# Performance work log

Measured on AMD Instinct MI355X. Metric: run time of the kernel, lower is better.

## Reference

```python
import jax, jax.numpy as jnp
import numpy as np

D = 256      # d_model
K = 8        # knn neighbors
Q = 2048     # num queries
N = 32768    # num superpoints
H = 8        # mamba heads (d_inner/head_dim)
HD = 64      # head_dim
ST = 64      # state_size
DIN = H * HD                 # 512, expand*d_model
CONV = DIN + 2 * ST          # 640
NPROJ = 2 * DIN + 2 * ST + H # 1160
HID = 1024   # ffn hidden
NL = 2       # ssm layers
KC = 4       # conv kernel


def _ln(x, eps=1e-5):
    m = x.mean(-1, keepdims=True)
    v = ((x - m) ** 2).mean(-1, keepdims=True)
    return (x - m) * jax.lax.rsqrt(v + eps)


def _silu(x):
    return x * jax.nn.sigmoid(x)


def _mamba2(x, Win, Wconv, bconv, A_log, Dh, dtb, rmsw, Wout):
    # x: [B, L, D]; faithful HF Mamba2Mixer recurrent form
    B, L, _ = x.shape
    proj = x @ Win.T  # [B,L,NPROJ]
    z, xBC, dt = jnp.split(proj, [DIN, DIN + CONV], axis=-1)
    # causal depthwise conv1d, kernel KC, left pad KC-1
    xp = jnp.pad(xBC, ((0, 0), (KC - 1, 0), (0, 0)))
    conv = sum(xp[:, j:j + L, :] * Wconv[:, j] for j in range(KC))
    xBC = _silu(conv + bconv)
    xs, Bm, Cm = jnp.split(xBC, [DIN, DIN + ST], axis=-1)
    dt = jax.nn.softplus(dt + dtb)  # [B,L,H]
    A = -jnp.exp(A_log)             # [H]
    xh = xs.reshape(B, L, H, HD)
    dA = jnp.exp(dt * A)            # [B,L,H]
    dBx = dt[..., None, None] * Bm[:, :, None, None, :] * xh[..., None]  # [B,L,H,HD,ST]

    def step(h, inp):
        dA_t, dBx_t, C_t = inp
        h = h * dA_t[..., None, None] + dBx_t
        y = jnp.einsum('bhds,bs->bhd', h, C_t)
        return h, y

    h0 = jnp.zeros((B, H, HD, ST), x.dtype)
    _, ys = jax.lax.scan(step, h0, (dA.transpose(1, 0, 2),
                                    dBx.transpose(1, 0, 2, 3, 4),
                                    Cm.transpose(1, 0, 2)))
    y = ys.transpose(1, 0, 2, 3) + Dh[None, None, :, None] * xh
    y = y.reshape(B, L, DIN) * _silu(z)  # gated RMSNorm
    y = y * jax.lax.rsqrt((y * y).mean(-1, keepdims=True) + 1e-5) * rmsw
    return y @ Wout.T


def setup_inputs() -> dict:
    key = jax.random.key(0)
    ks = jax.random.split(key, 32)
    s = 0.02
    rn = lambda i, sh: jax.random.normal(ks[i], sh, jnp.float32) * s
    inp = {
        'query': jax.random.normal(ks[0], (Q, D), jnp.float32),
        'query_pos': jax.random.uniform(ks[1], (Q, 3), jnp.float32),
        'inst_feats': jax.random.normal(ks[2], (N, D), jnp.float32),
        'sp_coords': jax.random.uniform(ks[3], (N, 3), jnp.float32),
        'w_q': rn(4, (D, D)), 'w_v': rn(5, (D, D)), 'w_o': rn(6, (D, D)),
        'w_k': rn(7, (K, D)), 'w_b': jnp.zeros((K,), jnp.float32),
        'ssm_Win': rn(8, (NL, NPROJ, D)),
        'ssm_Wconv': rn(9, (NL, CONV, KC)),
        'ssm_bconv': jnp.zeros((NL, CONV), jnp.float32),
        'ssm_Alog': jnp.log(jnp.broadcast_to(jnp.arange(1, H + 1, dtype=jnp.float32), (NL, H))),
        'ssm_D': jnp.ones((NL, H), jnp.float32),
        'ssm_dtb': jax.random.uniform(ks[10], (NL, H), jnp.float32) * 0.1,
        'ssm_rmsw': jnp.ones((NL, DIN), jnp.float32),
        'ssm_Wout': rn(11, (NL, D, DIN)),
        'ffn_w1': rn(12, (HID, D)), 'ffn_b1': jnp.zeros((HID,), jnp.float32),
        'ffn_w2': rn(13, (D, HID)), 'ffn_b2': jnp.zeros((D,), jnp.float32),
        'order': jnp.stack([jax.random.permutation(ks[14], Q),
                            jax.random.permutation(ks[15], Q)]).astype(jnp.int32),
    }
    return inp


def reference(query, query_pos, inst_feats, sp_coords,
              w_q, w_v, w_o, w_k, w_b,
              ssm_Win, ssm_Wconv, ssm_bconv, ssm_Alog, ssm_D, ssm_dtb, ssm_rmsw, ssm_Wout,
              ffn_w1, ffn_b1, ffn_w2, ffn_b2, order):
    # --- MambaAggregation: KNN group + small-K softmax mixing ---
    d2 = (query_pos ** 2).sum(-1, keepdims=True) + (sp_coords ** 2).sum(-1)[None, :] \
         - 2.0 * query_pos @ sp_coords.T  # [Q,N]
    _, idx = jax.lax.top_k(-d2, K)        # [Q,K] nearest neighbors
    feat = inst_feats[idx]                # [Q,K,D]
    q = query @ w_q.T
    v = feat @ w_v.T
    kw = jax.nn.softmax(q @ w_k.T + w_b, axis=-1)          # [Q,K]
    w = jnp.einsum('qk,qd,qkd->qd', kw, q, v)
    x = _ln(w @ w_o.T + query)

    # --- SSM: serialize along 2 orders, Mamba2 mix, unsort, average ---
    inv = jnp.argsort(order, axis=1)  # [2,Q]
    for l in range(NL):
        sc = x
        xn = _ln(x)
        xs = xn[order]  # [2,Q,D], two serialization paths as batch
        y = _mamba2(xs, ssm_Win[l], ssm_Wconv[l], ssm_bconv[l], ssm_Alog[l],
                    ssm_D[l], ssm_dtb[l], ssm_rmsw[l], ssm_Wout[l])
        back = jnp.take_along_axis(y, inv[:, :, None], axis=1)  # undo sort
        x = _ln(sc + back.mean(0))

    # --- FFN ---
    h = jax.nn.gelu(x @ ffn_w1.T + ffn_b1, approximate=False) @ ffn_w2.T + ffn_b2
    return _ln(x + h)
```

## Files before the change

kernel.cpp:

```cpp
#include <hip/hip_runtime.h>
#include <cstdint>


typedef __attribute__((ext_vector_type(8))) short bf16x8;
typedef __attribute__((ext_vector_type(4))) float f32x4;

__device__ __forceinline__ unsigned short f2bf(float f) {
  unsigned int u = __float_as_uint(f);
  u += 0x7fff + ((u >> 16) & 1);
  return (unsigned short)(u >> 16);
}
__device__ __forceinline__ float bf2f(unsigned short h) {
  return __uint_as_float(((unsigned int)h) << 16);
}

__global__ __launch_bounds__(256) void cvt_kernel(
    const float* __restrict__ src, unsigned short* __restrict__ hi,
    unsigned short* __restrict__ lo, int n4)
{
  const int i = blockIdx.x*256 + threadIdx.x;
  if (i < n4) {
    const float4 v = ((const float4*)src)[i];
    const unsigned short h0=f2bf(v.x), h1=f2bf(v.y), h2=f2bf(v.z), h3=f2bf(v.w);
    const unsigned short l0=f2bf(v.x-bf2f(h0)), l1=f2bf(v.y-bf2f(h1)),
                         l2=f2bf(v.z-bf2f(h2)), l3=f2bf(v.w-bf2f(h3));
    ((uint2*)hi)[i] = make_uint2((unsigned)h0 | ((unsigned)h1<<16),
                                 (unsigned)h2 | ((unsigned)h3<<16));
    ((uint2*)lo)[i] = make_uint2((unsigned)l0 | ((unsigned)l1<<16),
                                 (unsigned)l2 | ((unsigned)l3<<16));
  }
}

__device__ __forceinline__ bool flex_less(float d, int i, float dr, int ir) {
  return d < dr || (d == dr && i < ir);
}

#define KNN_INS_F(dv, iv)                                                      \
  do {                                                                         \
    const float _d = (dv); const int _v = (iv);                                \
    const bool a0 = _d < bd0;                                                  \
    const bool a1 = _d < bd1;                                                  \
    const bool a2 = _d < bd2;                                                  \
    const bool a3 = _d < bd3;                                                  \
    const bool a4 = _d < bd4;                                                  \
    const bool a5 = _d < bd5;                                                  \
    const bool a6 = _d < bd6;                                                  \
    bd7 = a6 ? bd6 : _d;              id7 = a6 ? id6 : _v;                     \
    bd6 = a5 ? bd5 : (a6 ? _d : bd6); id6 = a5 ? id5 : (a6 ? _v : id6);        \
    bd5 = a4 ? bd4 : (a5 ? _d : bd5); id5 = a4 ? id4 : (a5 ? _v : id5);        \
    bd4 = a3 ? bd3 : (a4 ? _d : bd4); id4 = a3 ? id3 : (a4 ? _v : id4);        \
    bd3 = a2 ? bd2 : (a3 ? _d : bd3); id3 = a2 ? id2 : (a3 ? _v : id3);        \
    bd2 = a1 ? bd1 : (a2 ? _d : bd2); id2 = a1 ? id1 : (a2 ? _v : id2);        \
    bd1 = a0 ? bd0 : (a1 ? _d : bd1); id1 = a0 ? id0 : (a1 ? _v : id1);        \
    bd0 = a0 ? _d : bd0;              id0 = a0 ? _v : id0;                     \
  } while (0)

#define KNN_INS_FLEX(dv, iv)                                                   \
  do {                                                                         \
    const float _d = (dv); const int _v = (iv);                                \
    const bool a0 = flex_less(_d, _v, bd0, id0);                               \
    const bool a1 = flex_less(_d, _v, bd1, id1);                               \
    const bool a2 = flex_less(_d, _v, bd2, id2);                               \
    const bool a3 = flex_less(_d, _v, bd3, id3);                               \
    const bool a4 = flex_less(_d, _v, bd4, id4);                               \
    const bool a5 = flex_less(_d, _v, bd5, id5);                               \
    const bool a6 = flex_less(_d, _v, bd6, id6);                               \
    bd7 = a6 ? bd6 : _d;              id7 = a6 ? id6 : _v;                     \
    bd6 = a5 ? bd5 : (a6 ? _d : bd6); id6 = a5 ? id5 : (a6 ? _v : id6);        \
    bd5 = a4 ? bd4 : (a5 ? _d : bd5); id5 = a4 ? id4 : (a5 ? _v : id5);        \
    bd4 = a3 ? bd3 : (a4 ? _d : bd4); id4 = a3 ? id3 : (a4 ? _v : id4);        \
    bd3 = a2 ? bd2 : (a3 ? _d : bd3); id3 = a2 ? id2 : (a3 ? _v : id3);        \
    bd2 = a1 ? bd1 : (a2 ? _d : bd2); id2 = a1 ? id1 : (a2 ? _v : id2);        \
    bd1 = a0 ? bd0 : (a1 ? _d : bd1); id1 = a0 ? id0 : (a1 ? _v : id1);        \
    bd0 = a0 ? _d : bd0;              id0 = a0 ? _v : id0;                     \
  } while (0)

#define KNN_RESET_F()                                                          \
  do {                                                                         \
    bd0=bd1=bd2=bd3=bd4=bd5=bd6=bd7 = 3.4e38f;                                 \
    id0=id1=id2=id3=id4=id5=id6=id7 = 0x7fffffff;                              \
  } while (0)

__global__ void prep_kernel(const float* __restrict__ spos,
                            float4* __restrict__ P4)
{
#pragma clang fp contract(off)
  const int n = blockIdx.x*256 + threadIdx.x;
  if (n < 32768) {
    const float sx = spos[n*3+0], sy = spos[n*3+1], sz = spos[n*3+2];
    P4[n] = make_float4(sx, sy, sz, sx*sx + sy*sy + sz*sz);
  }
}

__global__ __launch_bounds__(256) void knn_kernel(
    const float* __restrict__ qpos, const float4* __restrict__ P4,
    int* __restrict__ idx_out)
{
#pragma clang fp contract(off)
  __shared__ float skey[32];
  __shared__ int   sidx[32];
  const int q = blockIdx.x, tid = threadIdx.x;
  const int wave = tid >> 6, lane = tid & 63;
  const float qx = qpos[q*3+0], qy = qpos[q*3+1], qz = qpos[q*3+2];
  const float qq = qx*qx + qy*qy + qz*qz;
  float bd0,bd1,bd2,bd3,bd4,bd5,bd6,bd7;
  int   id0,id1,id2,id3,id4,id5,id6,id7;
  KNN_RESET_F();
  const float4* pp = P4 + (wave << 13) + lane;
  int nb = (wave << 13);
  for (int it = 0; it < 128; ++it) {
    const float4 p = *pp;  pp += 64;
    const float d2 = (qq + p.w) - 2.0f*(qx*p.x + qy*p.y + qz*p.z);
    unsigned long long m = __ballot(d2 < bd7);
    while (m) {
      const int l = __ffsll(m) - 1;
      m &= m - 1;
      const float dk = __shfl(d2, l);
      if (dk < bd7) KNN_INS_F(dk, nb + l);
    }
    nb += 64;
  }
  if (lane == 0) {
    const int o = wave*8;
    skey[o+0]=bd0; skey[o+1]=bd1; skey[o+2]=bd2; skey[o+3]=bd3;
    skey[o+4]=bd4; skey[o+5]=bd5; skey[o+6]=bd6; skey[o+7]=bd7;
    sidx[o+0]=id0; sidx[o+1]=id1; sidx[o+2]=id2; sidx[o+3]=id3;
    sidx[o+4]=id4; sidx[o+5]=id5; sidx[o+6]=id6; sidx[o+7]=id7;
  }
  __syncthreads();
  if (tid == 0) {
    KNN_RESET_F();
    for (int s = 0; s < 32; ++s) {
      const float dk = skey[s];
      const int   ui = sidx[s];
      if (flex_less(dk, ui, bd7, id7)) KNN_INS_FLEX(dk, ui);
    }
    idx_out[q*8+0]=id0; idx_out[q*8+1]=id1; idx_out[q*8+2]=id2; idx_out[q*8+3]=id3;
    idx_out[q*8+4]=id4; idx_out[q*8+5]=id5; idx_out[q*8+6]=id6; idx_out[q*8+7]=id7;
  }
}

__global__ void inv_kernel(const int* __restrict__ order, int* __restrict__ inv)
{
  int i = blockIdx.x*blockDim.x + threadIdx.x;
  if (i < 4096) { int b = i >> 11, t = i & 2047; inv[(b<<11) + order[i]] = t; }
}

#define GBM 128
#define GBN 128
#define GBK 32
#define GLDK 40
__global__ __launch_bounds__(256) void gemm_mfma(
    const unsigned short* __restrict__ Ahp, const unsigned short* __restrict__ Alp,
    const int* __restrict__ rowmap,
    const unsigned short* __restrict__ Bhp, const unsigned short* __restrict__ Blp,
    const float* __restrict__ bias,
    float* __restrict__ Y,
    unsigned short* __restrict__ Yh, unsigned short* __restrict__ Yl,
    int M, int Nn, int Kd, int act)
{
  __shared__ unsigned short Ah[GBM*GLDK], Al[GBM*GLDK];
  __shared__ unsigned short Bh[GBN*GLDK], Bl[GBN*GLDK];
  const int tid = threadIdx.x;
  const int bm = blockIdx.x, bn = blockIdx.y;
  const int wid = tid >> 6, lane = tid & 63;
  const int wr = wid >> 1, wc = wid & 1;
  const int l15 = lane & 15, lk = (lane >> 4) << 3;

  const int srow = tid >> 1, sk = (tid & 1) << 4;
  const int agrow = bm*GBM + srow;
  const int asrc = rowmap ? rowmap[agrow] : agrow;
  const unsigned short* ArH = Ahp + (size_t)asrc * Kd + sk;
  const unsigned short* ArL = Alp + (size_t)asrc * Kd + sk;
  const int wrow = bn*GBN + srow;
  const bool bok = (wrow < Nn);
  const unsigned short* BrH = Bhp + (size_t)(bok ? wrow : 0) * Kd + sk;
  const unsigned short* BrL = Blp + (size_t)(bok ? wrow : 0) * Kd + sk;

  f32x4 acc[4][4];
#pragma unroll
  for (int m = 0; m < 4; ++m)
#pragma unroll
    for (int n = 0; n < 4; ++n) acc[m][n] = (f32x4){0.f,0.f,0.f,0.f};

  const uint4 z4 = make_uint4(0u,0u,0u,0u);
  for (int k0 = 0; k0 < Kd; k0 += GBK) {
    const int so = srow*GLDK + sk;
    *(uint4*)&Ah[so]     = *(const uint4*)(ArH + k0);
    *(uint4*)&Ah[so + 8] = *(const uint4*)(ArH + k0 + 8);
    *(uint4*)&Al[so]     = *(const uint4*)(ArL + k0);
    *(uint4*)&Al[so + 8] = *(const uint4*)(ArL + k0 + 8);
    *(uint4*)&Bh[so]     = bok ? *(const uint4*)(BrH + k0)     : z4;
    *(uint4*)&Bh[so + 8] = bok ? *(const uint4*)(BrH + k0 + 8) : z4;
    *(uint4*)&Bl[so]     = bok ? *(const uint4*)(BrL + k0)     : z4;
    *(uint4*)&Bl[so + 8] = bok ? *(const uint4*)(BrL + k0 + 8) : z4;
    __syncthreads();
    bf16x8 afh[4], afl[4], bfh[4], bfl[4];
#pragma unroll
    for (int m = 0; m < 4; ++m) {
      const int row = wr*64 + m*16 + l15;
      afh[m] = *(const bf16x8*)&Ah[row*GLDK + lk];
      afl[m] = *(const bf16x8*)&Al[row*GLDK + lk];
    }
#pragma unroll
    for (int n = 0; n < 4; ++n) {
      const int row = wc*64 + n*16 + l15;
      bfh[n] = *(const bf16x8*)&Bh[row*GLDK + lk];
      bfl[n] = *(const bf16x8*)&Bl[row*GLDK + lk];
    }
#pragma unroll
    for (int m = 0; m < 4; ++m)
#pragma unroll
      for (int n = 0; n < 4; ++n) {
        acc[m][n] = __builtin_amdgcn_mfma_f32_16x16x32_bf16(afh[m], bfh[n], acc[m][n], 0,0,0);
        acc[m][n] = __builtin_amdgcn_mfma_f32_16x16x32_bf16(afh[m], bfl[n], acc[m][n], 0,0,0);
        acc[m][n] = __builtin_amdgcn_mfma_f32_16x16x32_bf16(afl[m], bfh[n], acc[m][n], 0,0,0);
      }
    __syncthreads();
  }
  const int crow0 = bm*GBM + wr*64 + (lane >> 4)*4;
#pragma unroll
  for (int m = 0; m < 4; ++m) {
#pragma unroll
    for (int n = 0; n < 4; ++n) {
      const int col = bn*GBN + wc*64 + n*16 + l15;
      if (col < Nn) {
#pragma unroll
        for (int r = 0; r < 4; ++r) {
          float v = acc[m][n][r];
          if (bias) v += bias[col];
          if (act == 1) v = 0.5f*v*(1.f + erff(v*0.7071067811865475f));
          const size_t idx = (size_t)(crow0 + m*16 + r)*Nn + col;
          if (Yh) {
            const unsigned short h = f2bf(v);
            Yh[idx] = h; Yl[idx] = f2bf(v - bf2f(h));
          } else {
            Y[idx] = v;
          }
        }
      }
    }
  }
}

__global__ __launch_bounds__(256) void kwmix_kernel(
    const float* __restrict__ QP, const float* __restrict__ wk,
    const float* __restrict__ wb, const float* __restrict__ V,
    unsigned short* __restrict__ Wh, unsigned short* __restrict__ Wl)
{
  const int wave = threadIdx.x >> 6, lane = threadIdx.x & 63;
  const int q = blockIdx.x*4 + wave;
  float qv[4];
#pragma unroll
  for (int j = 0; j < 4; ++j) qv[j] = QP[(size_t)q*256 + lane + 64*j];
  float logit[8];
#pragma unroll
  for (int k = 0; k < 8; ++k) {
    float p = 0.f;
#pragma unroll
    for (int j = 0; j < 4; ++j) p += qv[j]*wk[k*256 + lane + 64*j];
    for (int off = 32; off; off >>= 1) p += __shfl_xor(p, off);
    logit[k] = p + wb[k];
  }
  float mx = logit[0];
#pragma unroll
  for (int k = 1; k < 8; ++k) mx = fmaxf(mx, logit[k]);
  float e[8]; float s = 0.f;
#pragma unroll
  for (int k = 0; k < 8; ++k) { e[k] = expf(logit[k]-mx); s += e[k]; }
  float inv = 1.f/s;
  float acc[4] = {0.f,0.f,0.f,0.f};
#pragma unroll
  for (int k = 0; k < 8; ++k) {
    float kwv = e[k]*inv;
#pragma unroll
    for (int j = 0; j < 4; ++j)
      acc[j] = fmaf(kwv, V[(size_t)(q*8+k)*256 + lane + 64*j], acc[j]);
  }
#pragma unroll
  for (int j = 0; j < 4; ++j) {
    const float v = qv[j]*acc[j];
    const unsigned short h = f2bf(v);
    const size_t o = (size_t)q*256 + lane + 64*j;
    Wh[o] = h; Wl[o] = f2bf(v - bf2f(h));
  }
}

__global__ __launch_bounds__(256) void ln_kernel(
    const float* __restrict__ a, const float* __restrict__ b,
    float* __restrict__ out,
    unsigned short* __restrict__ oh, unsigned short* __restrict__ ol,
    int rows)
{
  const int wave = threadIdx.x >> 6, lane = threadIdx.x & 63;
  const int row = blockIdx.x*4 + wave;
  if (row >= rows) return;
  float v[4];
#pragma unroll
  for (int j = 0; j < 4; ++j) {
    float x = a[(size_t)row*256 + lane + 64*j];
    if (b) x += b[(size_t)row*256 + lane + 64*j];
    v[j] = x;
  }
  float s = v[0]+v[1]+v[2]+v[3];
  for (int off = 32; off; off >>= 1) s += __shfl_xor(s, off);
  float m = s * (1.0f/256.0f);
  float t = 0.f;
#pragma unroll
  for (int j = 0; j < 4; ++j) { float d = v[j]-m; t += d*d; }
  for (int off = 32; off; off >>= 1) t += __shfl_xor(t, off);
  float r = rsqrtf(t * (1.0f/256.0f) + 1e-5f);
#pragma unroll
  for (int j = 0; j < 4; ++j) {
    const float y = (v[j]-m)*r;
    const size_t o = (size_t)row*256 + lane + 64*j;
    if (out) out[o] = y;
    if (oh) { const unsigned short h = f2bf(y); oh[o] = h; ol[o] = f2bf(y - bf2f(h)); }
  }
}

__global__ __launch_bounds__(256) void ln_unsort_kernel(
    const float* __restrict__ OUTL, const int* __restrict__ INV,
    float* __restrict__ X,
    unsigned short* __restrict__ oh, unsigned short* __restrict__ ol)
{
  const int wave = threadIdx.x >> 6, lane = threadIdx.x & 63;
  const int q = blockIdx.x*4 + wave;
  const int i0 = INV[q], i1 = INV[2048 + q];
  float v[4];
#pragma unroll
  for (int j = 0; j < 4; ++j) {
    int d = lane + 64*j;
    v[j] = X[(size_t)q*256 + d]
         + 0.5f*(OUTL[(size_t)i0*256 + d] + OUTL[(size_t)(2048+i1)*256 + d]);
  }
  float s = v[0]+v[1]+v[2]+v[3];
  for (int off = 32; off; off >>= 1) s += __shfl_xor(s, off);
  float m = s * (1.0f/256.0f);
  float t = 0.f;
#pragma unroll
  for (int j = 0; j < 4; ++j) { float d = v[j]-m; t += d*d; }
  for (int off = 32; off; off >>= 1) t += __shfl_xor(t, off);
  float r = rsqrtf(t * (1.0f/256.0f) + 1e-5f);
#pragma unroll
  for (int j = 0; j < 4; ++j) {
    const float y = (v[j]-m)*r;
    const size_t o = (size_t)q*256 + lane + 64*j;
    X[o] = y;
    if (oh) { const unsigned short h = f2bf(y); oh[o] = h; ol[o] = f2bf(y - bf2f(h)); }
  }
}

__global__ void conv_kernel(const float* __restrict__ PROJ,
    const float* __restrict__ Wc, const float* __restrict__ bc,
    float* __restrict__ XBC)
{
  const int c = threadIdx.x;
  const int bt = blockIdx.x;
  const int t = bt & 2047;
  float acc = bc[c];
#pragma unroll
  for (int j = 0; j < 4; ++j) {
    int d = j - 3;
    if (t + d >= 0)
      acc = fmaf(PROJ[(size_t)(bt + d)*1160 + 512 + c], Wc[c*4+j], acc);
  }
  XBC[(size_t)bt*640 + c] = acc / (1.f + expf(-acc));
}

__global__ void dta_kernel(const float* __restrict__ PROJ,
    const float* __restrict__ dtb, const float* __restrict__ Alog,
    float* __restrict__ Ddt, float* __restrict__ Dda)
{
  const int i = blockIdx.x*256 + threadIdx.x;
  const int bt = i >> 3, hh = i & 7;
  float x = PROJ[(size_t)bt*1160 + 1152 + hh] + dtb[hh];
  float dt = (x > 20.f) ? x : log1pf(expf(x));
  float A = -expf(Alog[hh]);
  Ddt[hh*4096 + bt] = dt;
  Dda[hh*4096 + bt] = expf(dt * A);
}

__global__ __launch_bounds__(64) void scan1_kernel(
    const float* __restrict__ XBC, const float* __restrict__ Ddt,
    const float* __restrict__ Dda, float* __restrict__ SCH, float* __restrict__ PC)
{
  const int blk = blockIdx.x;
  const int c = blk & 31, hh = (blk >> 5) & 7, b = blk >> 8;
  const int lane = threadIdx.x;
  const int t0 = (b << 11) + (c << 6);
  __shared__ float Bsh[64][64];
  __shared__ float Xsh[64][64];
  __shared__ float dAs[64], dts[64];
#pragma unroll
  for (int it = 0; it < 16; ++it) {
    int idx = it*64 + lane;
    int t = idx >> 4, c4 = (idx & 15) << 2;
    *(float4*)&Bsh[t][c4] = *(const float4*)&XBC[(size_t)(t0 + t)*640 + 512 + c4];
    *(float4*)&Xsh[t][c4] = *(const float4*)&XBC[(size_t)(t0 + t)*640 + (hh<<6) + c4];
  }
  dAs[lane] = Dda[hh*4096 + t0 + lane];
  dts[lane] = Ddt[hh*4096 + t0 + lane];
  __syncthreads();
  float h[64];
#pragma unroll
  for (int s = 0; s < 64; ++s) h[s] = 0.f;
  float p = 1.f;
  for (int t = 0; t < 64; ++t) {
    const float dA = dAs[t];
    const float u = dts[t]*Xsh[t][lane];
    p *= dA;
    const float4* B4 = (const float4*)&Bsh[t][0];
#pragma unroll
    for (int s4 = 0; s4 < 16; ++s4) {
      float4 bv = B4[s4];
      h[4*s4+0] = fmaf(h[4*s4+0], dA, bv.x*u);
      h[4*s4+1] = fmaf(h[4*s4+1], dA, bv.y*u);
      h[4*s4+2] = fmaf(h[4*s4+2], dA, bv.z*u);
      h[4*s4+3] = fmaf(h[4*s4+3], dA, bv.w*u);
    }
  }
  float* op = SCH + (size_t)blk*4096 + lane*64;
#pragma unroll
  for (int s4 = 0; s4 < 16; ++s4)
    ((float4*)op)[s4] = make_float4(h[4*s4], h[4*s4+1], h[4*s4+2], h[4*s4+3]);
  if (lane == 0) PC[blk] = p;
}

__global__ void combine_kernel(float* __restrict__ SCH, const float* __restrict__ PC)
{
  const int tid = blockIdx.x*256 + threadIdx.x;
  const int bh = tid >> 12, ds = tid & 4095;
  float h = 0.f;
  for (int cc = 0; cc < 32; ++cc) {
    size_t o = ((size_t)(bh*32 + cc) << 12) + ds;
    float s = SCH[o];
    SCH[o] = h;
    h = fmaf(h, PC[bh*32+cc], s);
  }
}

__global__ __launch_bounds__(64) void scan2_kernel(
    const float* __restrict__ XBC, const float* __restrict__ Ddt,
    const float* __restrict__ Dda, const float* __restrict__ HST,
    const float* __restrict__ Dm, float* __restrict__ Yout)
{
  const int blk = blockIdx.x;
  const int c = blk & 31, hh = (blk >> 5) & 7, b = blk >> 8;
  const int lane = threadIdx.x;
  const int t0 = (b << 11) + (c << 6);
  __shared__ float Bsh[64][64];
  __shared__ float Csh[64][64];
  __shared__ float Xsh[64][64];
  __shared__ float dAs[64], dts[64];
#pragma unroll
  for (int it = 0; it < 16; ++it) {
    int idx = it*64 + lane;
    int t = idx >> 4, c4 = (idx & 15) << 2;
    *(float4*)&Bsh[t][c4] = *(const float4*)&XBC[(size_t)(t0 + t)*640 + 512 + c4];
    *(float4*)&Csh[t][c4] = *(const float4*)&XBC[(size_t)(t0 + t)*640 + 576 + c4];
    *(float4*)&Xsh[t][c4] = *(const float4*)&XBC[(size_t)(t0 + t)*640 + (hh<<6) + c4];
  }
  dAs[lane] = Dda[hh*4096 + t0 + lane];
  dts[lane] = Ddt[hh*4096 + t0 + lane];
  const float Dh = Dm[hh];
  float h[64];
  const float4* hp = (const float4*)(HST + (size_t)blk*4096 + lane*64);
#pragma unroll
  for (int s4 = 0; s4 < 16; ++s4) {
    float4 t4 = hp[s4];
    h[4*s4+0]=t4.x; h[4*s4+1]=t4.y; h[4*s4+2]=t4.z; h[4*s4+3]=t4.w;
  }
  __syncthreads();
  for (int t = 0; t < 64; ++t) {
    const float dA = dAs[t];
    const float u = dts[t]*Xsh[t][lane];
    float y = 0.f;
    const float4* B4 = (const float4*)&Bsh[t][0];
    const float4* C4 = (const float4*)&Csh[t][0];
#pragma unroll
    for (int s4 = 0; s4 < 16; ++s4) {
      float4 bv = B4[s4];
      float4 cv = C4[s4];
      h[4*s4+0] = fmaf(h[4*s4+0], dA, bv.x*u); y = fmaf(cv.x, h[4*s4+0], y);
      h[4*s4+1] = fmaf(h[4*s4+1], dA, bv.y*u); y = fmaf(cv.y, h[4*s4+1], y);
      h[4*s4+2] = fmaf(h[4*s4+2], dA, bv.z*u); y = fmaf(cv.z, h[4*s4+2], y);
      h[4*s4+3] = fmaf(h[4*s4+3], dA, bv.w*u); y = fmaf(cv.w, h[4*s4+3], y);
    }
    Yout[(size_t)(t0 + t)*512 + (hh<<6) + lane] = y + Dh*Xsh[t][lane];
  }
}

__global__ __launch_bounds__(256) void gaterms_kernel(
    const float* __restrict__ Y, const float* __restrict__ PROJ,
    const float* __restrict__ rmsw,
    unsigned short* __restrict__ Oh, unsigned short* __restrict__ Ol)
{
  const int wave = threadIdx.x >> 6, lane = threadIdx.x & 63;
  const int row = blockIdx.x*4 + wave;
  float v[8]; float ss = 0.f;
#pragma unroll
  for (int j = 0; j < 8; ++j) {
    float y = Y[(size_t)row*512 + lane + 64*j];
    float z = PROJ[(size_t)row*1160 + lane + 64*j];
    float g = y * (z / (1.f + expf(-z)));
    v[j] = g; ss += g*g;
  }
  for (int off = 32; off; off >>= 1) ss += __shfl_xor(ss, off);
  float r = rsqrtf(ss * (1.0f/512.0f) + 1e-5f);
#pragma unroll
  for (int j = 0; j < 8; ++j) {
    const float o = v[j] * r * rmsw[lane + 64*j];
    const unsigned short h = f2bf(o);
    const size_t ix = (size_t)row*512 + lane + 64*j;
    Oh[ix] = h; Ol[ix] = f2bf(o - bf2f(h));
  }
}

extern "C" void kernel_launch(void* const* d_in, const int* in_sizes, int n_in,
                              void* d_out, int out_size, void* d_ws, size_t ws_size,
                              hipStream_t stream)
{
  (void)in_sizes; (void)n_in; (void)out_size; (void)ws_size;
  const float* query = (const float*)d_in[0];
  const float* qpos  = (const float*)d_in[1];
  const float* feats = (const float*)d_in[2];
  const float* spos  = (const float*)d_in[3];
  const float* w_q   = (const float*)d_in[4];
  const float* w_v   = (const float*)d_in[5];
  const float* w_o   = (const float*)d_in[6];
  const float* w_k   = (const float*)d_in[7];
  const float* w_b   = (const float*)d_in[8];
  const float* Win   = (const float*)d_in[9];
  const float* Wconv = (const float*)d_in[10];
  const float* bconv = (const float*)d_in[11];
  const float* Alog  = (const float*)d_in[12];
  const float* Dm    = (const float*)d_in[13];
  const float* dtb   = (const float*)d_in[14];
  const float* rmsw  = (const float*)d_in[15];
  const float* Wout  = (const float*)d_in[16];
  const float* fw1   = (const float*)d_in[17];
  const float* fb1   = (const float*)d_in[18];
  const float* fw2   = (const float*)d_in[19];
  const float* fb2   = (const float*)d_in[20];
  const int*   order = (const int*)d_in[21];
  float* out = (float*)d_out;

  char* ws = (char*)d_ws;
  size_t off = 0;
  auto alloc = [&](size_t bytes) -> void* {
    void* p = ws + off;
    off = (off + bytes + 255) & ~(size_t)255;
    return p;
  };
  int*   IDX = (int*)alloc((size_t)2048*8*4);
  int*   INV = (int*)alloc((size_t)4096*4);
  float* PC  = (float*)alloc((size_t)512*4);
  float4* P4 = (float4*)alloc((size_t)32768*16);
  float* Ddt = (float*)alloc((size_t)4096*8*4);
  float* Dda = (float*)alloc((size_t)4096*8*4);
  float* QP  = (float*)alloc((size_t)2048*256*4);
  float* WO  = (float*)alloc((size_t)2048*256*4);
  float* X   = (float*)alloc((size_t)2048*256*4);
  float* U1  = (float*)alloc((size_t)4096*1160*4);
  float* U2  = (float*)alloc((size_t)4096*640*4);
  float* SCH = (float*)alloc((size_t)512*4096*4);
  float* Yb  = (float*)alloc((size_t)4096*512*4);
  float* U6  = (float*)alloc((size_t)4096*256*4);
  unsigned short* Qh  = (unsigned short*)alloc((size_t)2048*256*2);
  unsigned short* Ql  = (unsigned short*)alloc((size_t)2048*256*2);
  unsigned short* U7h = (unsigned short*)alloc((size_t)32768*256*2);
  unsigned short* U7l = (unsigned short*)alloc((size_t)32768*256*2);
  unsigned short* WBh = (unsigned short*)alloc((size_t)2048*256*2);
  unsigned short* WBl = (unsigned short*)alloc((size_t)2048*256*2);
  unsigned short* XNh = (unsigned short*)alloc((size_t)2048*256*2);
  unsigned short* XNl = (unsigned short*)alloc((size_t)2048*256*2);
  unsigned short* Ybh = (unsigned short*)alloc((size_t)4096*512*2);
  unsigned short* Ybl = (unsigned short*)alloc((size_t)4096*512*2);
  unsigned short* Xh  = (unsigned short*)alloc((size_t)2048*256*2);
  unsigned short* Xl  = (unsigned short*)alloc((size_t)2048*256*2);
  unsigned short* Wqh = (unsigned short*)alloc((size_t)256*256*2);
  unsigned short* Wql = (unsigned short*)alloc((size_t)256*256*2);
  unsigned short* Wvh = (unsigned short*)alloc((size_t)256*256*2);
  unsigned short* Wvl = (unsigned short*)alloc((size_t)256*256*2);
  unsigned short* Woh = (unsigned short*)alloc((size_t)256*256*2);
  unsigned short* Wol = (unsigned short*)alloc((size_t)256*256*2);
  unsigned short* Wih = (unsigned short*)alloc((size_t)2*1160*256*2);
  unsigned short* Wil = (unsigned short*)alloc((size_t)2*1160*256*2);
  unsigned short* Wuh = (unsigned short*)alloc((size_t)2*256*512*2);
  unsigned short* Wul = (unsigned short*)alloc((size_t)2*256*512*2);
  unsigned short* F1h = (unsigned short*)alloc((size_t)1024*256*2);
  unsigned short* F1l = (unsigned short*)alloc((size_t)1024*256*2);
  unsigned short* F2h = (unsigned short*)alloc((size_t)256*1024*2);
  unsigned short* F2l = (unsigned short*)alloc((size_t)256*1024*2);
  float* Vb   = U1;  float* PROJ = U1;
  float* XBC  = U2;
  float* OUTL = U6;  float* FFO  = U6;
  unsigned short* FFHh = U7h;
  unsigned short* FFHl = U7l;

  auto cvt = [&](const float* s, unsigned short* h, unsigned short* l, int n) {
    cvt_kernel<<<(n/4 + 255)/256, 256, 0, stream>>>(s, h, l, n/4);
  };

  inv_kernel<<<16, 256, 0, stream>>>(order, INV);
  prep_kernel<<<128, 256, 0, stream>>>(spos, P4);
  knn_kernel<<<2048, 256, 0, stream>>>(qpos, P4, IDX);
  cvt(query, Qh, Ql, 2048*256);
  cvt(feats, U7h, U7l, 32768*256);
  cvt(w_q, Wqh, Wql, 256*256);
  cvt(w_v, Wvh, Wvl, 256*256);
  cvt(w_o, Woh, Wol, 256*256);
  cvt(Win, Wih, Wil, 2*1160*256);
  cvt(Wout, Wuh, Wul, 2*256*512);
  cvt(fw1, F1h, F1l, 1024*256);
  cvt(fw2, F2h, F2l, 256*1024);
  gemm_mfma<<<dim3(16,2), 256, 0, stream>>>(Qh, Ql, nullptr, Wqh, Wql, nullptr,
                                            QP, nullptr, nullptr, 2048,256,256,0);
  gemm_mfma<<<dim3(128,2), 256, 0, stream>>>(U7h, U7l, IDX, Wvh, Wvl, nullptr,
                                             Vb, nullptr, nullptr, 16384,256,256,0);
  kwmix_kernel<<<512, 256, 0, stream>>>(QP, w_k, w_b, Vb, WBh, WBl);
  gemm_mfma<<<dim3(16,2), 256, 0, stream>>>(WBh, WBl, nullptr, Woh, Wol, nullptr,
                                            WO, nullptr, nullptr, 2048,256,256,0);
  ln_kernel<<<512, 256, 0, stream>>>(WO, query, X, nullptr, nullptr, 2048);

  for (int l = 0; l < 2; ++l) {
    ln_kernel<<<512, 256, 0, stream>>>(X, nullptr, nullptr, XNh, XNl, 2048);
    gemm_mfma<<<dim3(32,10), 256, 0, stream>>>(XNh, XNl, order,
                                               Wih + (size_t)l*1160*256,
                                               Wil + (size_t)l*1160*256,
                                               nullptr, PROJ, nullptr, nullptr,
                                               4096,1160,256,0);
    conv_kernel<<<4096, 640, 0, stream>>>(PROJ, Wconv + l*640*4, bconv + l*640, XBC);
    dta_kernel<<<128, 256, 0, stream>>>(PROJ, dtb + l*8, Alog + l*8, Ddt, Dda);
    scan1_kernel<<<512, 64, 0, stream>>>(XBC, Ddt, Dda, SCH, PC);
    combine_kernel<<<256, 256, 0, stream>>>(SCH, PC);
    scan2_kernel<<<512, 64, 0, stream>>>(XBC, Ddt, Dda, SCH, Dm + l*8, Yb);
    gaterms_kernel<<<1024, 256, 0, stream>>>(Yb, PROJ, rmsw + l*512, Ybh, Ybl);
    gemm_mfma<<<dim3(32,2), 256, 0, stream>>>(Ybh, Ybl, nullptr,
                                              Wuh + (size_t)l*256*512,
                                              Wul + (size_t)l*256*512,
                                              nullptr, OUTL, nullptr, nullptr,
                                              4096,256,512,0);
    ln_unsort_kernel<<<512, 256, 0, stream>>>(OUTL, INV, X,
                                              (l==1) ? Xh : nullptr,
                                              (l==1) ? Xl : nullptr);
  }

  gemm_mfma<<<dim3(16,8), 256, 0, stream>>>(Xh, Xl, nullptr, F1h, F1l, fb1,
                                            nullptr, FFHh, FFHl, 2048,1024,256,1);
  gemm_mfma<<<dim3(16,2), 256, 0, stream>>>(FFHh, FFHl, nullptr, F2h, F2l, fb2,
                                            FFO, nullptr, nullptr, 2048,256,1024,0);
  ln_kernel<<<512, 256, 0, stream>>>(FFO, X, out, nullptr, nullptr, 2048);
}
```

Before: 658.9 us.

## Mix gathered features before V projection and halve GEMM N-tile

Uses linearity to reorder the aggregation: instead of projecting all 16384 gathered neighbor features through w_v and then mixing, the softmax weights first mix the raw fp32 features per query, then a 2048-row GEMM applies w_v and multiplies elementwise by q in its epilogue. This removes the conversion of the full 32768x256 feature table and the 16384-row V GEMM. The GEMM N-tile also shrinks from 128 to 64, doubling the grid to improve occupancy on small GEMMs. The trade-off is reordered fp32 summation and a new epilogue multiply operand.

```diff
diff --git a/kernel.cpp b/kernel.cpp
--- a/kernel.cpp
+++ b/kernel.cpp
@@ -147,14 +147,14 @@
 }
 
 #define GBM 128
-#define GBN 128
+#define GBN 64
 #define GBK 32
 #define GLDK 40
 __global__ __launch_bounds__(256) void gemm_mfma(
     const unsigned short* __restrict__ Ahp, const unsigned short* __restrict__ Alp,
     const int* __restrict__ rowmap,
     const unsigned short* __restrict__ Bhp, const unsigned short* __restrict__ Blp,
-    const float* __restrict__ bias,
+    const float* __restrict__ bias, const float* __restrict__ emul,
     float* __restrict__ Y,
     unsigned short* __restrict__ Yh, unsigned short* __restrict__ Yl,
     int M, int Nn, int Kd, int act)
@@ -167,35 +167,35 @@
   const int wr = wid >> 1, wc = wid & 1;
   const int l15 = lane & 15, lk = (lane >> 4) << 3;
 
-  const int srow = tid >> 1, sk = (tid & 1) << 4;
-  const int agrow = bm*GBM + srow;
+  const int sar = tid >> 1, sak = (tid & 1) << 4;
+  const int agrow = bm*GBM + sar;
   const int asrc = rowmap ? rowmap[agrow] : agrow;
-  const unsigned short* ArH = Ahp + (size_t)asrc * Kd + sk;
-  const unsigned short* ArL = Alp + (size_t)asrc * Kd + sk;
-  const int wrow = bn*GBN + srow;
+  const unsigned short* ArH = Ahp + (size_t)asrc * Kd + sak;
+  const unsigned short* ArL = Alp + (size_t)asrc * Kd + sak;
+  const int sbr = tid >> 2, sbk = (tid & 3) << 3;
+  const int wrow = bn*GBN + sbr;
   const bool bok = (wrow < Nn);
-  const unsigned short* BrH = Bhp + (size_t)(bok ? wrow : 0) * Kd + sk;
-  const unsigned short* BrL = Blp + (size_t)(bok ? wrow : 0) * Kd + sk;
-
-  f32x4 acc[4][4];
+  const unsigned short* BrH = Bhp + (size_t)(bok ? wrow : 0) * Kd + sbk;
+  const unsigned short* BrL = Blp + (size_t)(bok ? wrow : 0) * Kd + sbk;
+
+  f32x4 acc[4][2];
 #pragma unroll
   for (int m = 0; m < 4; ++m)
 #pragma unroll
-    for (int n = 0; n < 4; ++n) acc[m][n] = (f32x4){0.f,0.f,0.f,0.f};
+    for (int n = 0; n < 2; ++n) acc[m][n] = (f32x4){0.f,0.f,0.f,0.f};
 
   const uint4 z4 = make_uint4(0u,0u,0u,0u);
   for (int k0 = 0; k0 < Kd; k0 += GBK) {
-    const int so = srow*GLDK + sk;
-    *(uint4*)&Ah[so]     = *(const uint4*)(ArH + k0);
-    *(uint4*)&Ah[so + 8] = *(const uint4*)(ArH + k0 + 8);
-    *(uint4*)&Al[so]     = *(const uint4*)(ArL + k0);
-    *(uint4*)&Al[so + 8] = *(const uint4*)(ArL + k0 + 8);
-    *(uint4*)&Bh[so]     = bok ? *(const uint4*)(BrH + k0)     : z4;
-    *(uint4*)&Bh[so + 8] = bok ? *(const uint4*)(BrH + k0 + 8) : z4;
-    *(uint4*)&Bl[so]     = bok ? *(const uint4*)(BrL + k0)     : z4;
-    *(uint4*)&Bl[so + 8] = bok ? *(const uint4*)(BrL + k0 + 8) : z4;
+    const int ao = sar*GLDK + sak;
+    *(uint4*)&Ah[ao]     = *(const uint4*)(ArH + k0);
+    *(uint4*)&Ah[ao + 8] = *(const uint4*)(ArH + k0 + 8);
+    *(uint4*)&Al[ao]     = *(const uint4*)(ArL + k0);
+    *(uint4*)&Al[ao + 8] = *(const uint4*)(ArL + k0 + 8);
+    const int bo = sbr*GLDK + sbk;
+    *(uint4*)&Bh[bo] = bok ? *(const uint4*)(BrH + k0) : z4;
+    *(uint4*)&Bl[bo] = bok ? *(const uint4*)(BrL + k0) : z4;
     __syncthreads();
-    bf16x8 afh[4], afl[4], bfh[4], bfl[4];
+    bf16x8 afh[4], afl[4], bfh[2], bfl[2];
 #pragma unroll
     for (int m = 0; m < 4; ++m) {
       const int row = wr*64 + m*16 + l15;
@@ -203,15 +203,15 @@
       afl[m] = *(const bf16x8*)&Al[row*GLDK + lk];
     }
 #pragma unroll
-    for (int n = 0; n < 4; ++n) {
-      const int row = wc*64 + n*16 + l15;
+    for (int n = 0; n < 2; ++n) {
+      const int row = wc*32 + n*16 + l15;
       bfh[n] = *(const bf16x8*)&Bh[row*GLDK + lk];
       bfl[n] = *(const bf16x8*)&Bl[row*GLDK + lk];
     }
 #pragma unroll
     for (int m = 0; m < 4; ++m)
 #pragma unroll
-      for (int n = 0; n < 4; ++n) {
+      for (int n = 0; n < 2; ++n) {
         acc[m][n] = __builtin_amdgcn_mfma_f32_16x16x32_bf16(afh[m], bfh[n], acc[m][n], 0,0,0);
         acc[m][n] = __builtin_amdgcn_mfma_f32_16x16x32_bf16(afh[m], bfl[n], acc[m][n], 0,0,0);
         acc[m][n] = __builtin_amdgcn_mfma_f32_16x16x32_bf16(afl[m], bfh[n], acc[m][n], 0,0,0);
@@ -222,8 +222,8 @@
 #pragma unroll
   for (int m = 0; m < 4; ++m) {
 #pragma unroll
-    for (int n = 0; n < 4; ++n) {
-      const int col = bn*GBN + wc*64 + n*16 + l15;
+    for (int n = 0; n < 2; ++n) {
+      const int col = bn*GBN + wc*32 + n*16 + l15;
       if (col < Nn) {
 #pragma unroll
         for (int r = 0; r < 4; ++r) {
@@ -231,6 +231,7 @@
           if (bias) v += bias[col];
           if (act == 1) v = 0.5f*v*(1.f + erff(v*0.7071067811865475f));
           const size_t idx = (size_t)(crow0 + m*16 + r)*Nn + col;
+          if (emul) v *= emul[idx];
           if (Yh) {
             const unsigned short h = f2bf(v);
             Yh[idx] = h; Yl[idx] = f2bf(v - bf2f(h));
@@ -243,10 +244,11 @@
   }
 }
 
-__global__ __launch_bounds__(256) void kwmix_kernel(
+__global__ __launch_bounds__(256) void kwmix2_kernel(
     const float* __restrict__ QP, const float* __restrict__ wk,
-    const float* __restrict__ wb, const float* __restrict__ V,
-    unsigned short* __restrict__ Wh, unsigned short* __restrict__ Wl)
+    const float* __restrict__ wb, const float* __restrict__ feats,
+    const int* __restrict__ IDX,
+    unsigned short* __restrict__ Fh, unsigned short* __restrict__ Fl)
 {
   const int wave = threadIdx.x >> 6, lane = threadIdx.x & 63;
   const int q = blockIdx.x*4 + wave;
@@ -272,17 +274,17 @@
   float acc[4] = {0.f,0.f,0.f,0.f};
 #pragma unroll
   for (int k = 0; k < 8; ++k) {
-    float kwv = e[k]*inv;
+    const float kwv = e[k]*inv;
+    const int ii = IDX[q*8+k];
 #pragma unroll
     for (int j = 0; j < 4; ++j)
-      acc[j] = fmaf(kwv, V[(size_t)(q*8+k)*256 + lane + 64*j], acc[j]);
+      acc[j] = fmaf(kwv, feats[(size_t)ii*256 + lane + 64*j], acc[j]);
   }
 #pragma unroll
   for (int j = 0; j < 4; ++j) {
-    const float v = qv[j]*acc[j];
-    const unsigned short h = f2bf(v);
+    const unsigned short h = f2bf(acc[j]);
     const size_t o = (size_t)q*256 + lane + 64*j;
-    Wh[o] = h; Wl[o] = f2bf(v - bf2f(h));
+    Fh[o] = h; Fl[o] = f2bf(acc[j] - bf2f(h));
   }
 }
 
@@ -569,8 +571,8 @@
   float* U6  = (float*)alloc((size_t)4096*256*4);
   unsigned short* Qh  = (unsigned short*)alloc((size_t)2048*256*2);
   unsigned short* Ql  = (unsigned short*)alloc((size_t)2048*256*2);
-  unsigned short* U7h = (unsigned short*)alloc((size_t)32768*256*2);
-  unsigned short* U7l = (unsigned short*)alloc((size_t)32768*256*2);
+  unsigned short* U7h = (unsigned short*)alloc((size_t)2048*1024*2);
+  unsigned short* U7l = (unsigned short*)alloc((size_t)2048*1024*2);
   unsigned short* WBh = (unsigned short*)alloc((size_t)2048*256*2);
   unsigned short* WBl = (unsigned short*)alloc((size_t)2048*256*2);
   unsigned short* XNh = (unsigned short*)alloc((size_t)2048*256*2);
@@ -593,7 +595,7 @@
   unsigned short* F1l = (unsigned short*)alloc((size_t)1024*256*2);
   unsigned short* F2h = (unsigned short*)alloc((size_t)256*1024*2);
   unsigned short* F2l = (unsigned short*)alloc((size_t)256*1024*2);
-  float* Vb   = U1;  float* PROJ = U1;
+  float* PROJ = U1;
   float* XBC  = U2;
   float* OUTL = U6;  float* FFO  = U6;
   unsigned short* FFHh = U7h;
@@ -607,7 +609,6 @@
   prep_kernel<<<128, 256, 0, stream>>>(spos, P4);
   knn_kernel<<<2048, 256, 0, stream>>>(qpos, P4, IDX);
   cvt(query, Qh, Ql, 2048*256);
-  cvt(feats, U7h, U7l, 32768*256);
   cvt(w_q, Wqh, Wql, 256*256);
   cvt(w_v, Wvh, Wvl, 256*256);
   cvt(w_o, Woh, Wol, 256*256);
@@ -615,21 +616,25 @@
   cvt(Wout, Wuh, Wul, 2*256*512);
   cvt(fw1, F1h, F1l, 1024*256);
   cvt(fw2, F2h, F2l, 256*1024);
-  gemm_mfma<<<dim3(16,2), 256, 0, stream>>>(Qh, Ql, nullptr, Wqh, Wql, nullptr,
-                                            QP, nullptr, nullptr, 2048,256,256,0);
-  gemm_mfma<<<dim3(128,2), 256, 0, stream>>>(U7h, U7l, IDX, Wvh, Wvl, nullptr,
-                                             Vb, nullptr, nullptr, 16384,256,256,0);
-  kwmix_kernel<<<512, 256, 0, stream>>>(QP, w_k, w_b, Vb, WBh, WBl);
-  gemm_mfma<<<dim3(16,2), 256, 0, stream>>>(WBh, WBl, nullptr, Woh, Wol, nullptr,
-                                            WO, nullptr, nullptr, 2048,256,256,0);
+  gemm_mfma<<<dim3(16,4), 256, 0, stream>>>(Qh, Ql, nullptr, Wqh, Wql, nullptr,
+                                            nullptr, QP, nullptr, nullptr,
+                                            2048,256,256,0);
+  kwmix2_kernel<<<512, 256, 0, stream>>>(QP, w_k, w_b, feats, IDX, XNh, XNl);
+  gemm_mfma<<<dim3(16,4), 256, 0, stream>>>(XNh, XNl, nullptr, Wvh, Wvl, nullptr,
+                                            QP, nullptr, WBh, WBl,
+                                            2048,256,256,0);
+  gemm_mfma<<<dim3(16,4), 256, 0, stream>>>(WBh, WBl, nullptr, Woh, Wol, nullptr,
+                                            nullptr, WO, nullptr, nullptr,
+                                            2048,256,256,0);
   ln_kernel<<<512, 256, 0, stream>>>(WO, query, X, nullptr, nullptr, 2048);
 
   for (int l = 0; l < 2; ++l) {
     ln_kernel<<<512, 256, 0, stream>>>(X, nullptr, nullptr, XNh, XNl, 2048);
-    gemm_mfma<<<dim3(32,10), 256, 0, stream>>>(XNh, XNl, order,
+    gemm_mfma<<<dim3(32,19), 256, 0, stream>>>(XNh, XNl, order,
                                                Wih + (size_t)l*1160*256,
                                                Wil + (size_t)l*1160*256,
-                                               nullptr, PROJ, nullptr, nullptr,
+                                               nullptr, nullptr, PROJ,
+                                               nullptr, nullptr,
                                                4096,1160,256,0);
     conv_kernel<<<4096, 640, 0, stream>>>(PROJ, Wconv + l*640*4, bconv + l*640, XBC);
     dta_kernel<<<128, 256, 0, stream>>>(PROJ, dtb + l*8, Alog + l*8, Ddt, Dda);
@@ -637,19 +642,22 @@
     combine_kernel<<<256, 256, 0, stream>>>(SCH, PC);
     scan2_kernel<<<512, 64, 0, stream>>>(XBC, Ddt, Dda, SCH, Dm + l*8, Yb);
     gaterms_kernel<<<1024, 256, 0, stream>>>(Yb, PROJ, rmsw + l*512, Ybh, Ybl);
-    gemm_mfma<<<dim3(32,2), 256, 0, stream>>>(Ybh, Ybl, nullptr,
+    gemm_mfma<<<dim3(32,4), 256, 0, stream>>>(Ybh, Ybl, nullptr,
                                               Wuh + (size_t)l*256*512,
                                               Wul + (size_t)l*256*512,
-                                              nullptr, OUTL, nullptr, nullptr,
+                                              nullptr, nullptr, OUTL,
+                                              nullptr, nullptr,
                                               4096,256,512,0);
     ln_unsort_kernel<<<512, 256, 0, stream>>>(OUTL, INV, X,
                                               (l==1) ? Xh : nullptr,
                                               (l==1) ? Xl : nullptr);
   }
 
-  gemm_mfma<<<dim3(16,8), 256, 0, stream>>>(Xh, Xl, nullptr, F1h, F1l, fb1,
-                                            nullptr, FFHh, FFHl, 2048,1024,256,1);
-  gemm_mfma<<<dim3(16,2), 256, 0, stream>>>(FFHh, FFHl, nullptr, F2h, F2l, fb2,
-                                            FFO, nullptr, nullptr, 2048,256,1024,0);
+  gemm_mfma<<<dim3(16,16), 256, 0, stream>>>(Xh, Xl, nullptr, F1h, F1l, fb1,
+                                             nullptr, nullptr, FFHh, FFHl,
+                                             2048,1024,256,1);
+  gemm_mfma<<<dim3(16,4), 256, 0, stream>>>(FFHh, FFHl, nullptr, F2h, F2l, fb2,
+                                            nullptr, FFO, nullptr, nullptr,
+                                            2048,256,1024,0);
   ln_kernel<<<512, 256, 0, stream>>>(FFO, X, out, nullptr, nullptr, 2048);
 }
```

After: 584.0 us. 1.13x faster.
